# Kernel tuning notes

Measured on AMD Instinct MI355X. Metric: run time of the kernel, lower is better.

## Reference

```python
import jax, jax.numpy as jnp
import numpy as np

N_FEAT = 256
NUM_HEADS = 8
EPS = 1e-12  # torch F.normalize default eps


def setup_inputs() -> dict:
    key = jax.random.key(0)
    k1, k2, k3 = jax.random.split(key, 3)
    b, c, h, w = 1, N_FEAT, 64, 64
    x = jax.random.normal(k1, (b, c, h, w), dtype=jnp.float32)
    # 1x1 convs == channel GEMMs; store as (out_ch, in_ch) matrices
    w_qkv = jax.random.normal(k2, (3 * c, c), dtype=jnp.float32) * (1.0 / np.sqrt(c))
    w_proj = jax.random.normal(k3, (c, c), dtype=jnp.float32) * (1.0 / np.sqrt(c))
    temperature = jnp.ones((NUM_HEADS, 1, 1), dtype=jnp.float32)
    return {"x": x, "w_qkv": w_qkv, "w_proj": w_proj, "temperature": temperature}


def _l2norm(t):
    n = jnp.linalg.norm(t, axis=-1, keepdims=True)
    return t / jnp.maximum(n, EPS)


def reference(x, w_qkv, w_proj, temperature):
    b, c, h, w = x.shape
    heads = temperature.shape[0]
    d = c // heads
    hw = h * w
    xf = x.reshape(b, c, hw)
    # qkv 1x1 conv: (b, 3c, hw)
    qkv = jnp.einsum('oc,bcs->bos', w_qkv, xf)
    qkv = qkv.reshape(b, 3, heads, d, hw)
    q, k, v = qkv[:, 0], qkv[:, 1], qkv[:, 2]  # (b, heads, d, hw)
    q = jnp.swapaxes(q, -2, -1)  # (b, heads, hw, d)
    k = jnp.swapaxes(k, -2, -1)
    v = jnp.swapaxes(v, -2, -1)
    q = _l2norm(q)
    k = _l2norm(k)
    attn = jnp.einsum('bhsd,bhtd->bhst', q, k) * temperature[None]  # (b, heads, hw, hw)
    attn = jax.nn.softmax(attn, axis=-1)
    out = jnp.einsum('bhst,bhtd->bhsd', attn, v)  # (b, heads, hw, d)
    # faithful to torch: permute(0,2,1,3).reshape(b,c,h,w)
    out = out.transpose(0, 2, 1, 3).reshape(b, c, h, w)
    out = jnp.einsum('oc,bchw->bohw', w_proj, out)
    return out
```

## Files before the change

kernel.cpp:

```cpp
#include <hip/hip_runtime.h>
#include <stdint.h>

#define HW 4096
#define NH 8
#define NSPLIT 4
#define TSPLIT (HW / NSPLIT)

typedef __attribute__((ext_vector_type(8))) short short8;
typedef __attribute__((ext_vector_type(4))) short s4b;
typedef __attribute__((ext_vector_type(4))) float floatx4;

__device__ inline float bf2f(uint16_t u) {
  union { uint32_t i; float f; } v; v.i = ((uint32_t)u) << 16; return v.f;
}
__device__ inline float bflo(uint32_t u) {
  union { uint32_t i; float f; } v; v.i = u << 16; return v.f;
}
__device__ inline float bfhi(uint32_t u) {
  union { uint32_t i; float f; } v; v.i = u & 0xFFFF0000u; return v.f;
}
__device__ inline uint16_t f2bf(float f) {
  union { float f; uint32_t i; } v; v.f = f;
  uint32_t u = v.i; u += 0x7fffu + ((u >> 16) & 1u); return (uint16_t)(u >> 16);
}
__device__ inline uint32_t pk2(float a, float b) {
  return (uint32_t)f2bf(a) | ((uint32_t)f2bf(b) << 16);
}
__device__ inline uint32_t asu(float f) { union { float f; uint32_t i; } v; v.f = f; return v.i; }
__device__ inline uint32_t pk2r(float a, float b) {
#if __has_builtin(__builtin_amdgcn_cvt_pk_bf16_f32)
  union { short2 s; uint32_t u; } x;
  x.s = __builtin_amdgcn_cvt_pk_bf16_f32(a, b);
  return x.u;
#else
  return __builtin_amdgcn_perm(asu(b) + 0x8000u, asu(a) + 0x8000u, 0x07060302u);
#endif
}
__device__ inline s4b mk_s4(uint32_t lo, uint32_t hi) {
  union { uint32_t u[2]; s4b s; } x; x.u[0] = lo; x.u[1] = hi; return x.s;
}
__device__ inline floatx4 mfma16(s4b a, s4b b, floatx4 c) {
#if __has_builtin(__builtin_amdgcn_mfma_f32_16x16x16bf16_1k)
  return __builtin_amdgcn_mfma_f32_16x16x16bf16_1k(a, b, c, 0, 0, 0);
#else
  floatx4 d = c;
  asm volatile("v_mfma_f32_16x16x16_bf16 %0, %1, %2, %0" : "+v"(d) : "v"(a), "v"(b));
  return d;
#endif
}
__device__ inline bool is_f32(const uint32_t* Tp32) { return (Tp32[0] & 0xFFFFu) == 0u; }
__device__ inline float read_temp(const void* Tp, int h) {
  if (is_f32((const uint32_t*)Tp)) return ((const float*)Tp)[h];
  return bf2f(((const uint16_t*)Tp)[h]);
}

__global__ __launch_bounds__(256) void k_gemm_qkv(const void* __restrict__ X,
                                                  const void* __restrict__ A,
                                                  const void* __restrict__ Tp,
                                                  uint16_t* __restrict__ Qr,
                                                  uint16_t* __restrict__ Kr,
                                                  uint16_t* __restrict__ Vr) {
  __shared__ uint16_t sA[128 * 64];
  __shared__ uint16_t sB[32 * 64];
  __shared__ uint16_t sXr[64 * 34];
  int tid = threadIdx.x;
  int w = tid >> 6, lane = tid & 63, lm = lane & 15, qd = lane >> 4;
  int n0 = blockIdx.x * 32, m0 = blockIdx.y * 128;
  bool aF32 = is_f32((const uint32_t*)Tp);
  floatx4 acc[2][2];
#pragma unroll
  for (int i = 0; i < 2; ++i)
#pragma unroll
    for (int j = 0; j < 2; ++j) acc[i][j] = (floatx4){0.f, 0.f, 0.f, 0.f};

  for (int k0 = 0; k0 < 256; k0 += 64) {
    __syncthreads();
    {
      int cl = tid >> 2, sc = (tid & 3) * 8;
      uint32_t* l32 = (uint32_t*)sXr;
      int base = cl * 17 + (sc >> 1);
      if (aF32) {
        const float4* x4 = (const float4*)((const float*)X + (k0 + cl) * HW + n0 + sc);
        float4 a = x4[0], b = x4[1];
        l32[base + 0] = pk2(a.x, a.y); l32[base + 1] = pk2(a.z, a.w);
        l32[base + 2] = pk2(b.x, b.y); l32[base + 3] = pk2(b.z, b.w);
      } else {
        uint4 a = *(const uint4*)((const uint16_t*)X + (k0 + cl) * HW + n0 + sc);
        l32[base + 0] = a.x; l32[base + 1] = a.y;
        l32[base + 2] = a.z; l32[base + 3] = a.w;
      }
    }
#pragma unroll
    for (int r = 0; r < 4; ++r) {
      int ch = r * 256 + tid; int row = ch >> 3, c8 = ch & 7;
      uint4 v;
      if (aF32) {
        const float4* s4 = (const float4*)((const float*)A + (m0 + row) * 256 + k0 + c8 * 8);
        float4 a = s4[0], b = s4[1];
        v = make_uint4(pk2(a.x, a.y), pk2(a.z, a.w), pk2(b.x, b.y), pk2(b.z, b.w));
      } else {
        v = *(const uint4*)((const uint16_t*)A + (m0 + row) * 256 + k0 + c8 * 8);
      }
      *(uint4*)(&sA[row * 64 + (c8 ^ (row & 7)) * 8]) = v;
    }
    __syncthreads();
    {
      int sl = tid >> 3, cs = (tid & 7) * 8;
      uint32_t wb[4];
#pragma unroll
      for (int j = 0; j < 4; ++j) {
        uint32_t lo = sXr[(cs + 2 * j) * 34 + sl];
        uint32_t hi = sXr[(cs + 2 * j + 1) * 34 + sl];
        wb[j] = lo | (hi << 16);
      }
      *(uint4*)(&sB[sl * 64 + (((cs >> 3) ^ (sl & 7))) * 8]) =
          make_uint4(wb[0], wb[1], wb[2], wb[3]);
    }
    __syncthreads();
#pragma unroll
    for (int kk = 0; kk < 2; ++kk) {
      short8 af[2];
#pragma unroll
      for (int mt = 0; mt < 2; ++mt) {
        int row = w * 32 + mt * 16 + lm;
        af[mt] = *(const short8*)(&sA[row * 64 + ((kk * 4 + qd) ^ (row & 7)) * 8]);
      }
#pragma unroll
      for (int nt = 0; nt < 2; ++nt) {
        int row = nt * 16 + lm;
        short8 bf = *(const short8*)(&sB[row * 64 + ((kk * 4 + qd) ^ (row & 7)) * 8]);
#pragma unroll
        for (int mt = 0; mt < 2; ++mt)
          acc[mt][nt] = __builtin_amdgcn_mfma_f32_16x16x32_bf16(af[mt], bf, acc[mt][nt], 0, 0, 0);
      }
    }
  }
  int ow = m0 + w * 32;
  int type = ow >> 8;
  int hh = (ow >> 5) & 7;
  float tv = read_temp(Tp, hh);
#pragma unroll
  for (int nt = 0; nt < 2; ++nt) {
    int s = n0 + nt * 16 + lm;
    if (type < 2) {
      float ssq = 0.f;
#pragma unroll
      for (int mt = 0; mt < 2; ++mt)
#pragma unroll
        for (int r = 0; r < 4; ++r) ssq += acc[mt][nt][r] * acc[mt][nt][r];
      ssq += __shfl_xor(ssq, 16, 64);
      ssq += __shfl_xor(ssq, 32, 64);
      float sc = (type == 0 ? tv : 1.0f) / fmaxf(sqrtf(ssq), 1e-12f);
      uint16_t* dst = (type == 0 ? Qr : Kr) + ((hh << 12) + s) * 32;
#pragma unroll
      for (int mt = 0; mt < 2; ++mt)
        *(uint2*)(dst + mt * 16 + qd * 4) =
            make_uint2(pk2r(acc[mt][nt][0] * sc, acc[mt][nt][1] * sc),
                       pk2r(acc[mt][nt][2] * sc, acc[mt][nt][3] * sc));
    } else {
#pragma unroll
      for (int mt = 0; mt < 2; ++mt)
#pragma unroll
        for (int r = 0; r < 4; ++r)
          Vr[(hh * 32 + mt * 16 + qd * 4 + r) * HW + s] = f2bf(acc[mt][nt][r]);
    }
  }
}

__global__ __launch_bounds__(256, 4) void k_attn(const uint16_t* __restrict__ Qr,
                                                 const uint16_t* __restrict__ Kr,
                                                 const uint16_t* __restrict__ Vr,
                                                 const void* __restrict__ Tp,
                                                 uint16_t* __restrict__ Op,
                                                 float* __restrict__ Lp) {
  __shared__ uint16_t sK[256 * 32];
  __shared__ uint16_t sV[32 * 256];
  int tid = threadIdx.x;
  int w = tid >> 6, lane = tid & 63, lm = lane & 15, qd = lane >> 4;
  int bid = blockIdx.x;
  int h = bid & 7;
  int j = bid >> 3;
  int sp = j & 3;
  int qb = j >> 2;
  int srow = qb * 128 + w * 32;
  const float c1 = 1.44269504088896340736f;
  float c2 = fabsf(read_temp(Tp, h)) * c1;
  short8 qf0 = *(const short8*)(Qr + ((h << 12) + srow + lm) * 32 + qd * 8);
  short8 qf1 = *(const short8*)(Qr + ((h << 12) + srow + 16 + lm) * 32 + qd * 8);
  const uint16_t* Kg = Kr + (h << 12) * 32;
  const uint16_t* Vg = Vr + (h * 32) * HW;
  floatx4 o00 = {0.f, 0.f, 0.f, 0.f}, o01 = {0.f, 0.f, 0.f, 0.f};
  floatx4 o10 = {0.f, 0.f, 0.f, 0.f}, o11 = {0.f, 0.f, 0.f, 0.f};
  floatx4 l0 = {0.f, 0.f, 0.f, 0.f}, l1 = {0.f, 0.f, 0.f, 0.f};
  const s4b ones = mk_s4(0x3F803F80u, 0x3F803F80u);

  int rK = tid >> 2, cK = tid & 3;
  uint16_t* dk0 = &sK[rK * 32 + (cK ^ ((rK >> 1) & 3)) * 8];
  const uint16_t* gk0 = Kg + (sp * TSPLIT + rK) * 32 + cK * 8;
  int dVb = tid >> 5, cVx = tid & 31;
  int s0x = dVb >> 1;
  bool sw = dVb & 1;
  uint16_t* dv0 = &sV[dVb * 256 + (cVx ^ s0x) * 8];
  uint16_t* dv1 = &sV[(dVb + 8) * 256 + (cVx ^ s0x ^ 4) * 8];
  const uint16_t* gv0 = Vg + dVb * HW + sp * TSPLIT + cVx * 8;

  uint4 rk0 = *(const uint4*)gk0;
  uint4 rk1 = *(const uint4*)(gk0 + 2048);
  uint4 rk2 = *(const uint4*)(gk0 + 4096);
  uint4 rk3 = *(const uint4*)(gk0 + 6144);
  uint4 rv0 = *(const uint4*)gv0;
  uint4 rv1 = *(const uint4*)(gv0 + 8 * HW);
  uint4 rv2 = *(const uint4*)(gv0 + 16 * HW);
  uint4 rv3 = *(const uint4*)(gv0 + 24 * HW);

  for (int i = 0; i < TSPLIT / 256; ++i) {
    __syncthreads();
    *(uint4*)dk0 = rk0;
    *(uint4*)(dk0 + 2048) = rk1;
    *(uint4*)(dk0 + 4096) = rk2;
    *(uint4*)(dk0 + 6144) = rk3;
    *(uint4*)dv0 = sw ? make_uint4(rv0.z, rv0.w, rv0.x, rv0.y) : rv0;
    *(uint4*)(dv0 + 4096) = sw ? make_uint4(rv2.z, rv2.w, rv2.x, rv2.y) : rv2;
    *(uint4*)dv1 = sw ? make_uint4(rv1.z, rv1.w, rv1.x, rv1.y) : rv1;
    *(uint4*)(dv1 + 4096) = sw ? make_uint4(rv3.z, rv3.w, rv3.x, rv3.y) : rv3;
    if (i + 1 < TSPLIT / 256) {
      gk0 += 256 * 32; gv0 += 256;
      rk0 = *(const uint4*)gk0;
      rk1 = *(const uint4*)(gk0 + 2048);
      rk2 = *(const uint4*)(gk0 + 4096);
      rk3 = *(const uint4*)(gk0 + 6144);
      rv0 = *(const uint4*)gv0;
      rv1 = *(const uint4*)(gv0 + 8 * HW);
      rv2 = *(const uint4*)(gv0 + 16 * HW);
      rv3 = *(const uint4*)(gv0 + 24 * HW);
    }
    asm volatile("s_waitcnt lgkmcnt(0)\n\ts_barrier" ::: "memory");
#pragma unroll
    for (int nt = 0; nt < 16; ++nt) {
      int krow = nt * 16 + lm;
      short8 kf = *(const short8*)(&sK[krow * 32 + (qd ^ ((lm >> 1) & 3)) * 8]);
      int gp = (nt * 4 + qd) ^ lm;
      s4b v0 = *(const s4b*)(&sV[lm * 256 + gp * 4]);
      s4b v1 = *(const s4b*)(&sV[(lm + 16) * 256 + gp * 4]);
      floatx4 z = {0.f, 0.f, 0.f, 0.f};
      floatx4 sv = __builtin_amdgcn_mfma_f32_16x16x32_bf16(kf, qf0, z, 0, 0, 0);
      float p0 = __builtin_amdgcn_exp2f(fmaf(sv[0], c1, -c2));
      float p1 = __builtin_amdgcn_exp2f(fmaf(sv[1], c1, -c2));
      float p2 = __builtin_amdgcn_exp2f(fmaf(sv[2], c1, -c2));
      float p3 = __builtin_amdgcn_exp2f(fmaf(sv[3], c1, -c2));
      s4b pa = mk_s4(pk2r(p0, p1), pk2r(p2, p3));
      o00 = mfma16(pa, v0, o00);
      o01 = mfma16(pa, v1, o01);
      l0 = mfma16(pa, ones, l0);
      sv = __builtin_amdgcn_mfma_f32_16x16x32_bf16(kf, qf1, z, 0, 0, 0);
      p0 = __builtin_amdgcn_exp2f(fmaf(sv[0], c1, -c2));
      p1 = __builtin_amdgcn_exp2f(fmaf(sv[1], c1, -c2));
      p2 = __builtin_amdgcn_exp2f(fmaf(sv[2], c1, -c2));
      p3 = __builtin_amdgcn_exp2f(fmaf(sv[3], c1, -c2));
      pa = mk_s4(pk2r(p0, p1), pk2r(p2, p3));
      o10 = mfma16(pa, v0, o10);
      o11 = mfma16(pa, v1, o11);
      l1 = mfma16(pa, ones, l1);
    }
  }
  int sb = (sp * NH + h) * HW + srow;
  uint16_t* op = Op + (size_t)sb * 32;
#pragma unroll
  for (int r = 0; r < 4; ++r) {
    op[(qd * 4 + r) * 32 + lm] = f2bf(o00[r]);
    op[(qd * 4 + r) * 32 + 16 + lm] = f2bf(o01[r]);
    op[(16 * 32) + (qd * 4 + r) * 32 + lm] = f2bf(o10[r]);
    op[(16 * 32) + (qd * 4 + r) * 32 + 16 + lm] = f2bf(o11[r]);
  }
  if (lm == 0) {
#pragma unroll
    for (int r = 0; r < 4; ++r) {
      Lp[sb + qd * 4 + r] = l0[r];
      Lp[sb + 16 + qd * 4 + r] = l1[r];
    }
  }
}

__global__ __launch_bounds__(256) void k_gemm_proj(const void* __restrict__ A,
                                                   const uint16_t* __restrict__ Op,
                                                   const float* __restrict__ Lp,
                                                   void* __restrict__ C,
                                                   const uint32_t* __restrict__ Tp32) {
  __shared__ uint16_t sA[64 * 64];
  __shared__ uint16_t sB[32 * 64];
  __shared__ float sOp[64 * 33];
  int tid = threadIdx.x;
  int w = tid >> 6, lane = tid & 63, lm = lane & 15, qd = lane >> 4;
  int n0 = blockIdx.x * 32, m0 = blockIdx.y * 64;
  int h = (n0 >> 5) & 7, slo = n0 >> 8;
  bool aF32 = is_f32(Tp32);
  floatx4 acc[2];
  acc[0] = (floatx4){0.f, 0.f, 0.f, 0.f};
  acc[1] = (floatx4){0.f, 0.f, 0.f, 0.f};
  int cl = tid >> 2, dp = (tid & 3) * 8;
  int dd = tid >> 3, spart = (tid & 7) * 8;

  for (int k0 = 0; k0 < 256; k0 += 64) {
    __syncthreads();
#pragma unroll
    for (int r = 0; r < 2; ++r) {
      int ch = r * 256 + tid; int row = ch >> 3, c8 = ch & 7;
      uint4 v;
      if (aF32) {
        const float4* s4 = (const float4*)((const float*)A + (m0 + row) * 256 + k0 + c8 * 8);
        float4 a = s4[0], b = s4[1];
        v = make_uint4(pk2(a.x, a.y), pk2(a.z, a.w), pk2(b.x, b.y), pk2(b.z, b.w));
      } else {
        v = *(const uint4*)((const uint16_t*)A + (m0 + row) * 256 + k0 + c8 * 8);
      }
      *(uint4*)(&sA[row * 64 + (c8 ^ (row & 7)) * 8]) = v;
    }
    {
      int s = slo + 16 * (k0 + cl);
      float L = 0.f;
      float a[8];
#pragma unroll
      for (int q = 0; q < 8; ++q) a[q] = 0.f;
#pragma unroll
      for (int sp = 0; sp < NSPLIT; ++sp) {
        size_t gj = (size_t)(sp * NH + h) * HW + s;
        L += Lp[gj];
        uint4 x = *(const uint4*)(Op + gj * 32 + dp);
        a[0] += bflo(x.x); a[1] += bfhi(x.x); a[2] += bflo(x.y); a[3] += bfhi(x.y);
        a[4] += bflo(x.z); a[5] += bfhi(x.z); a[6] += bflo(x.w); a[7] += bfhi(x.w);
      }
      float inv = __builtin_amdgcn_rcpf(L);
#pragma unroll
      for (int q = 0; q < 8; ++q) sOp[cl * 33 + dp + q] = a[q] * inv;
    }
    __syncthreads();
    {
      float b[8];
#pragma unroll
      for (int q = 0; q < 8; ++q) b[q] = sOp[(spart + q) * 33 + dd];
      *(uint4*)(&sB[dd * 64 + ((spart >> 3) ^ (dd & 7)) * 8]) =
          make_uint4(pk2r(b[0], b[1]), pk2r(b[2], b[3]),
                     pk2r(b[4], b[5]), pk2r(b[6], b[7]));
    }
    __syncthreads();
#pragma unroll
    for (int kk = 0; kk < 2; ++kk) {
      int arow = w * 16 + lm;
      short8 af = *(const short8*)(&sA[arow * 64 + ((kk * 4 + qd) ^ (arow & 7)) * 8]);
#pragma unroll
      for (int nt = 0; nt < 2; ++nt) {
        int row = nt * 16 + lm;
        short8 bf = *(const short8*)(&sB[row * 64 + ((kk * 4 + qd) ^ (row & 7)) * 8]);
        acc[nt] = __builtin_amdgcn_mfma_f32_16x16x32_bf16(af, bf, acc[nt], 0, 0, 0);
      }
    }
  }
  bool f32o = is_f32(Tp32);
#pragma unroll
  for (int nt = 0; nt < 2; ++nt)
#pragma unroll
    for (int r = 0; r < 4; ++r) {
      int row = m0 + w * 16 + qd * 4 + r;
      int col = n0 + nt * 16 + lm;
      if (f32o) ((float*)C)[row * HW + col] = acc[nt][r];
      else ((uint16_t*)C)[row * HW + col] = f2bf(acc[nt][r]);
    }
}

extern "C" void kernel_launch(void* const* d_in, const int* in_sizes, int n_in,
                              void* d_out, int out_size, void* d_ws, size_t ws_size,
                              hipStream_t stream) {
  const void* X  = d_in[0];
  const void* Wq = d_in[1];
  const void* Wp = d_in[2];
  const void* Tp = d_in[3];
  const uint32_t* Tp32 = (const uint32_t*)Tp;
  uint16_t* ws = (uint16_t*)d_ws;
  uint16_t* Qr = ws;
  uint16_t* Kr = Qr + NH * HW * 32;
  uint16_t* Vr = Kr + NH * HW * 32;
  uint16_t* Op = Vr + NH * 32 * HW;
  float* Lp = (float*)(Op + (size_t)NSPLIT * NH * HW * 32);

  k_gemm_qkv<<<dim3(128, 6), 256, 0, stream>>>(X, Wq, Tp, Qr, Kr, Vr);
  k_attn<<<dim3(1024), 256, 0, stream>>>(Qr, Kr, Vr, Tp, Op, Lp);
  k_gemm_proj<<<dim3(128, 4), 256, 0, stream>>>(Wp, Op, Lp, d_out, Tp32);
}
```

Baseline: 114.4 us.

## Use 16x16x32 MFMA for PV, fold log2e into Q, bias via accumulator init

```diff
diff --git a/kernel.cpp b/kernel.cpp
--- a/kernel.cpp
+++ b/kernel.cpp
@@ -7,7 +7,6 @@
 #define TSPLIT (HW / NSPLIT)
 
 typedef __attribute__((ext_vector_type(8))) short short8;
-typedef __attribute__((ext_vector_type(4))) short s4b;
 typedef __attribute__((ext_vector_type(4))) float floatx4;
 
 __device__ inline float bf2f(uint16_t u) {
@@ -22,9 +21,6 @@
 __device__ inline uint16_t f2bf(float f) {
   union { float f; uint32_t i; } v; v.f = f;
   uint32_t u = v.i; u += 0x7fffu + ((u >> 16) & 1u); return (uint16_t)(u >> 16);
-}
-__device__ inline uint32_t pk2(float a, float b) {
-  return (uint32_t)f2bf(a) | ((uint32_t)f2bf(b) << 16);
 }
 __device__ inline uint32_t asu(float f) { union { float f; uint32_t i; } v; v.f = f; return v.i; }
 __device__ inline uint32_t pk2r(float a, float b) {
@@ -36,17 +32,9 @@
   return __builtin_amdgcn_perm(asu(b) + 0x8000u, asu(a) + 0x8000u, 0x07060302u);
 #endif
 }
-__device__ inline s4b mk_s4(uint32_t lo, uint32_t hi) {
-  union { uint32_t u[2]; s4b s; } x; x.u[0] = lo; x.u[1] = hi; return x.s;
-}
-__device__ inline floatx4 mfma16(s4b a, s4b b, floatx4 c) {
-#if __has_builtin(__builtin_amdgcn_mfma_f32_16x16x16bf16_1k)
-  return __builtin_amdgcn_mfma_f32_16x16x16bf16_1k(a, b, c, 0, 0, 0);
-#else
-  floatx4 d = c;
-  asm volatile("v_mfma_f32_16x16x16_bf16 %0, %1, %2, %0" : "+v"(d) : "v"(a), "v"(b));
-  return d;
-#endif
+__device__ inline short8 mk_s8(uint32_t a, uint32_t b, uint32_t c, uint32_t d) {
+  union { uint32_t u[4]; short8 s; } x;
+  x.u[0] = a; x.u[1] = b; x.u[2] = c; x.u[3] = d; return x.s;
 }
 __device__ inline bool is_f32(const uint32_t* Tp32) { return (Tp32[0] & 0xFFFFu) == 0u; }
 __device__ inline float read_temp(const void* Tp, int h) {
@@ -82,8 +70,8 @@
       if (aF32) {
         const float4* x4 = (const float4*)((const float*)X + (k0 + cl) * HW + n0 + sc);
         float4 a = x4[0], b = x4[1];
-        l32[base + 0] = pk2(a.x, a.y); l32[base + 1] = pk2(a.z, a.w);
-        l32[base + 2] = pk2(b.x, b.y); l32[base + 3] = pk2(b.z, b.w);
+        l32[base + 0] = pk2r(a.x, a.y); l32[base + 1] = pk2r(a.z, a.w);
+        l32[base + 2] = pk2r(b.x, b.y); l32[base + 3] = pk2r(b.z, b.w);
       } else {
         uint4 a = *(const uint4*)((const uint16_t*)X + (k0 + cl) * HW + n0 + sc);
         l32[base + 0] = a.x; l32[base + 1] = a.y;
@@ -97,7 +85,7 @@
       if (aF32) {
         const float4* s4 = (const float4*)((const float*)A + (m0 + row) * 256 + k0 + c8 * 8);
         float4 a = s4[0], b = s4[1];
-        v = make_uint4(pk2(a.x, a.y), pk2(a.z, a.w), pk2(b.x, b.y), pk2(b.z, b.w));
+        v = make_uint4(pk2r(a.x, a.y), pk2r(a.z, a.w), pk2r(b.x, b.y), pk2r(b.z, b.w));
       } else {
         v = *(const uint4*)((const uint16_t*)A + (m0 + row) * 256 + k0 + c8 * 8);
       }
@@ -150,7 +138,8 @@
         for (int r = 0; r < 4; ++r) ssq += acc[mt][nt][r] * acc[mt][nt][r];
       ssq += __shfl_xor(ssq, 16, 64);
       ssq += __shfl_xor(ssq, 32, 64);
-      float sc = (type == 0 ? tv : 1.0f) / fmaxf(sqrtf(ssq), 1e-12f);
+      float sc = (type == 0 ? tv * 1.44269504088896340736f : 1.0f) /
+                 fmaxf(sqrtf(ssq), 1e-12f);
       uint16_t* dst = (type == 0 ? Qr : Kr) + ((hh << 12) + s) * 32;
 #pragma unroll
       for (int mt = 0; mt < 2; ++mt)
@@ -192,7 +181,9 @@
   floatx4 o00 = {0.f, 0.f, 0.f, 0.f}, o01 = {0.f, 0.f, 0.f, 0.f};
   floatx4 o10 = {0.f, 0.f, 0.f, 0.f}, o11 = {0.f, 0.f, 0.f, 0.f};
   floatx4 l0 = {0.f, 0.f, 0.f, 0.f}, l1 = {0.f, 0.f, 0.f, 0.f};
-  const s4b ones = mk_s4(0x3F803F80u, 0x3F803F80u);
+  const short8 ones8 = mk_s8(0x3F803F80u, 0x3F803F80u, 0x3F803F80u, 0x3F803F80u);
+  const floatx4 zb = {-c2, -c2, -c2, -c2};
+  const int kswz = (qd ^ ((lm >> 1) & 3)) * 8;
 
   int rK = tid >> 2, cK = tid & 3;
   uint16_t* dk0 = &sK[rK * 32 + (cK ^ ((rK >> 1) & 3)) * 8];
@@ -236,35 +227,41 @@
     }
     asm volatile("s_waitcnt lgkmcnt(0)\n\ts_barrier" ::: "memory");
 #pragma unroll
-    for (int nt = 0; nt < 16; ++nt) {
-      int krow = nt * 16 + lm;
-      short8 kf = *(const short8*)(&sK[krow * 32 + (qd ^ ((lm >> 1) & 3)) * 8]);
-      int gp = (nt * 4 + qd) ^ lm;
-      s4b v0 = *(const s4b*)(&sV[lm * 256 + gp * 4]);
-      s4b v1 = *(const s4b*)(&sV[(lm + 16) * 256 + gp * 4]);
-      floatx4 z = {0.f, 0.f, 0.f, 0.f};
-      floatx4 sv = __builtin_amdgcn_mfma_f32_16x16x32_bf16(kf, qf0, z, 0, 0, 0);
-      float p0 = __builtin_amdgcn_exp2f(fmaf(sv[0], c1, -c2));
-      float p1 = __builtin_amdgcn_exp2f(fmaf(sv[1], c1, -c2));
-      float p2 = __builtin_amdgcn_exp2f(fmaf(sv[2], c1, -c2));
-      float p3 = __builtin_amdgcn_exp2f(fmaf(sv[3], c1, -c2));
-      s4b pa = mk_s4(pk2r(p0, p1), pk2r(p2, p3));
-      o00 = mfma16(pa, v0, o00);
-      o01 = mfma16(pa, v1, o01);
-      l0 = mfma16(pa, ones, l0);
-      sv = __builtin_amdgcn_mfma_f32_16x16x32_bf16(kf, qf1, z, 0, 0, 0);
-      p0 = __builtin_amdgcn_exp2f(fmaf(sv[0], c1, -c2));
-      p1 = __builtin_amdgcn_exp2f(fmaf(sv[1], c1, -c2));
-      p2 = __builtin_amdgcn_exp2f(fmaf(sv[2], c1, -c2));
-      p3 = __builtin_amdgcn_exp2f(fmaf(sv[3], c1, -c2));
-      pa = mk_s4(pk2r(p0, p1), pk2r(p2, p3));
-      o10 = mfma16(pa, v0, o10);
-      o11 = mfma16(pa, v1, o11);
-      l1 = mfma16(pa, ones, l1);
-    }
-  }
-  int sb = (sp * NH + h) * HW + srow;
-  uint16_t* op = Op + (size_t)sb * 32;
+    for (int nt = 0; nt < 8; ++nt) {
+      short8 kfa = *(const short8*)(&sK[(nt * 32 + lm) * 32 + kswz]);
+      short8 kfb = *(const short8*)(&sK[(nt * 32 + 16 + lm) * 32 + kswz]);
+      int gpa = (nt * 8 + qd) ^ lm;
+      int gpb = (nt * 8 + 4 + qd) ^ lm;
+      uint2 va0 = *(const uint2*)(&sV[lm * 256 + gpa * 4]);
+      uint2 vb0 = *(const uint2*)(&sV[lm * 256 + gpb * 4]);
+      uint2 va1 = *(const uint2*)(&sV[(lm + 16) * 256 + gpa * 4]);
+      uint2 vb1 = *(const uint2*)(&sV[(lm + 16) * 256 + gpb * 4]);
+      short8 vv0 = mk_s8(va0.x, va0.y, vb0.x, vb0.y);
+      short8 vv1 = mk_s8(va1.x, va1.y, vb1.x, vb1.y);
+      floatx4 sa = __builtin_amdgcn_mfma_f32_16x16x32_bf16(kfa, qf0, zb, 0, 0, 0);
+      floatx4 sb = __builtin_amdgcn_mfma_f32_16x16x32_bf16(kfb, qf0, zb, 0, 0, 0);
+      short8 pa = mk_s8(
+          pk2r(__builtin_amdgcn_exp2f(sa[0]), __builtin_amdgcn_exp2f(sa[1])),
+          pk2r(__builtin_amdgcn_exp2f(sa[2]), __builtin_amdgcn_exp2f(sa[3])),
+          pk2r(__builtin_amdgcn_exp2f(sb[0]), __builtin_amdgcn_exp2f(sb[1])),
+          pk2r(__builtin_amdgcn_exp2f(sb[2]), __builtin_amdgcn_exp2f(sb[3])));
+      o00 = __builtin_amdgcn_mfma_f32_16x16x32_bf16(pa, vv0, o00, 0, 0, 0);
+      o01 = __builtin_amdgcn_mfma_f32_16x16x32_bf16(pa, vv1, o01, 0, 0, 0);
+      l0  = __builtin_amdgcn_mfma_f32_16x16x32_bf16(pa, ones8, l0, 0, 0, 0);
+      sa = __builtin_amdgcn_mfma_f32_16x16x32_bf16(kfa, qf1, zb, 0, 0, 0);
+      sb = __builtin_amdgcn_mfma_f32_16x16x32_bf16(kfb, qf1, zb, 0, 0, 0);
+      pa = mk_s8(
+          pk2r(__builtin_amdgcn_exp2f(sa[0]), __builtin_amdgcn_exp2f(sa[1])),
+          pk2r(__builtin_amdgcn_exp2f(sa[2]), __builtin_amdgcn_exp2f(sa[3])),
+          pk2r(__builtin_amdgcn_exp2f(sb[0]), __builtin_amdgcn_exp2f(sb[1])),
+          pk2r(__builtin_amdgcn_exp2f(sb[2]), __builtin_amdgcn_exp2f(sb[3])));
+      o10 = __builtin_amdgcn_mfma_f32_16x16x32_bf16(pa, vv0, o10, 0, 0, 0);
+      o11 = __builtin_amdgcn_mfma_f32_16x16x32_bf16(pa, vv1, o11, 0, 0, 0);
+      l1  = __builtin_amdgcn_mfma_f32_16x16x32_bf16(pa, ones8, l1, 0, 0, 0);
+    }
+  }
+  int sb_ = (sp * NH + h) * HW + srow;
+  uint16_t* op = Op + (size_t)sb_ * 32;
 #pragma unroll
   for (int r = 0; r < 4; ++r) {
     op[(qd * 4 + r) * 32 + lm] = f2bf(o00[r]);
@@ -275,8 +272,8 @@
   if (lm == 0) {
 #pragma unroll
     for (int r = 0; r < 4; ++r) {
-      Lp[sb + qd * 4 + r] = l0[r];
-      Lp[sb + 16 + qd * 4 + r] = l1[r];
+      Lp[sb_ + qd * 4 + r] = l0[r];
+      Lp[sb_ + 16 + qd * 4 + r] = l1[r];
     }
   }
 }
@@ -309,7 +306,7 @@
       if (aF32) {
         const float4* s4 = (const float4*)((const float*)A + (m0 + row) * 256 + k0 + c8 * 8);
         float4 a = s4[0], b = s4[1];
-        v = make_uint4(pk2(a.x, a.y), pk2(a.z, a.w), pk2(b.x, b.y), pk2(b.z, b.w));
+        v = make_uint4(pk2r(a.x, a.y), pk2r(a.z, a.w), pk2r(b.x, b.y), pk2r(b.z, b.w));
       } else {
         v = *(const uint4*)((const uint16_t*)A + (m0 + row) * 256 + k0 + c8 * 8);
       }
```

Result: faster. 109.6 us (-4.2%).
